# Kernel optimization log

Hardware: AMD Instinct MI355X
Metric: run time of the kernel (lower is better)

Reference implementation:

```python
import jax, jax.numpy as jnp
import numpy as np

N_NODES = 100000
N_EDGES = 1000000
F_IN = 64
F_HID = 32


def setup_inputs() -> dict:
    key = jax.random.key(0)
    k = jax.random.split(key, 6)
    x = jax.random.normal(k[0], (N_NODES, F_IN), dtype=jnp.float32)
    edge_index = jax.random.randint(k[1], (2, N_EDGES), 0, N_NODES, dtype=jnp.int32)
    # Glorot-ish scaled weights (PyG GCNConv linear has no bias; bias added post-aggregation)
    W1 = jax.random.normal(k[2], (F_IN, F_HID), dtype=jnp.float32) / np.sqrt(F_IN)
    b1 = jax.random.normal(k[3], (F_HID,), dtype=jnp.float32) * 0.01
    W2 = jax.random.normal(k[4], (F_HID, F_IN), dtype=jnp.float32) / np.sqrt(F_HID)
    b2 = jax.random.normal(k[5], (F_IN,), dtype=jnp.float32) * 0.01
    return {"x": x, "edge_index": edge_index, "W1": W1, "b1": b1, "W2": W2, "b2": b2}


def gcn_conv(x, W, b, src, dst, n):
    """PyG GCNConv: h = x @ W; add self-loops; symmetric norm; scatter-add; + bias."""
    h = x @ W  # [N, out]
    ones = jnp.ones(src.shape[0], dtype=h.dtype)
    # degree includes the implicit self-loop (+1 per node)
    deg = jax.ops.segment_sum(ones, dst, num_segments=n) + 1.0  # [N]
    dis = jax.lax.rsqrt(deg)  # deg^{-1/2}
    norm = dis[src] * dis[dst]  # [E]
    agg = jax.ops.segment_sum(h[src] * norm[:, None], dst, num_segments=n)
    # self-loop contribution: norm_ii = deg_i^{-1}
    agg = agg + h * (dis * dis)[:, None]
    return agg + b


def reference(x, edge_index, W1, b1, W2, b2):
    src, dst = edge_index[0], edge_index[1]
    n = x.shape[0]
    h = jax.nn.relu(gcn_conv(x, W1, b1, src, dst, n))
    # dropout is identity in eval mode
    return gcn_conv(h, W2, b2, src, dst, n)
```

## Files before the change

### kernel.cpp

```cpp
#include <hip/hip_runtime.h>
#include <hip/hip_fp16.h>

#define NN 100000
#define NE 1000000
#define FIN 64
#define FHID 32
#define NB 782
#define BNODES 128
#define NCH 256
#define CH ((NE + NCH - 1) / NCH)
#define GEMB ((NN + 31) / 32)

union H8 { __half2 h2[4]; float4 f4; };
union H4 { __half2 h2[2]; float2 f2; };

__global__ __launch_bounds__(256) void k_bhist(const int* __restrict__ dst, int* __restrict__ phist) {
    __shared__ int lh[NB];
    for (int i = threadIdx.x; i < NB; i += 256) lh[i] = 0;
    __syncthreads();
    int k = blockIdx.x;
    int e0 = k * CH, e1 = min(e0 + CH, NE);
    for (int e = e0 + threadIdx.x; e < e1; e += 256) atomicAdd(&lh[dst[e] >> 7], 1);
    __syncthreads();
    for (int b = threadIdx.x; b < NB; b += 256) phist[(size_t)k * NB + b] = lh[b];
}

__global__ __launch_bounds__(256) void k_bscan(int* __restrict__ phist, int* __restrict__ btot) {
    int b = blockIdx.x;
    int k = threadIdx.x;
    int v = phist[(size_t)k * NB + b];
    int lane = k & 63, wv = k >> 6;
    int incl = v;
#pragma unroll
    for (int s = 1; s < 64; s <<= 1) {
        int t = __shfl_up(incl, s, 64);
        if (lane >= s) incl += t;
    }
    __shared__ int wt[4];
    if (lane == 63) wt[wv] = incl;
    __syncthreads();
    int add = 0;
#pragma unroll
    for (int w = 0; w < 4; ++w) add += (w < wv) ? wt[w] : 0;
    phist[(size_t)k * NB + b] = add + incl - v;
    if (k == 255) btot[b] = add + incl;
}

__global__ __launch_bounds__(1024) void k_bbase(const int* __restrict__ btot, int* __restrict__ bbase,
                                                int* __restrict__ off) {
    __shared__ int s[1024];
    int b = threadIdx.x;
    int v = (b < NB) ? btot[b] : 0;
    s[b] = v;
    __syncthreads();
    for (int d = 1; d < 1024; d <<= 1) {
        int t = (b >= d) ? s[b - d] : 0;
        __syncthreads();
        s[b] += t;
        __syncthreads();
    }
    if (b < NB) bbase[b] = s[b] - v;
    if (b == 0) { bbase[NB] = NE; off[NN] = NE; }
}

__global__ __launch_bounds__(256) void k_scatter_gemm1(const int* __restrict__ ei,
                                                       const int* __restrict__ phist,
                                                       const int* __restrict__ bbase,
                                                       int* __restrict__ ebuf,
                                                       const float* __restrict__ x,
                                                       const float* __restrict__ W1,
                                                       __half* __restrict__ h1) {
    int r = blockIdx.x;
    bool issc;
    int id;
    if (r < 2 * NCH) { issc = !(r & 1); id = r >> 1; }
    else             { issc = false;    id = r - NCH; }
    if (issc) {
        __shared__ int lh[NB];
        __shared__ int lbase[NB];
        int k = id;
        for (int b = threadIdx.x; b < NB; b += 256) {
            lh[b] = 0;
            lbase[b] = bbase[b] + phist[(size_t)k * NB + b];
        }
        __syncthreads();
        int e0 = k * CH, e1 = min(e0 + CH, NE);
        for (int e = e0 + threadIdx.x; e < e1; e += 256) {
            int s = ei[e], d = ei[NE + e];
            int bb = d >> 7;
            int rr = atomicAdd(&lh[bb], 1);
            ebuf[lbase[bb] + rr] = s * BNODES + (d & 127);
        }
        return;
    }
    __shared__ float Wl[FIN * FHID];
    for (int t = threadIdx.x; t < FIN * FHID / 4; t += 256)
        reinterpret_cast<float4*>(Wl)[t] = reinterpret_cast<const float4*>(W1)[t];
    __syncthreads();
    int row = id * 32 + (threadIdx.x >> 3);
    int l = threadIdx.x & 7;
    if (row >= NN) return;
    const float4* xr = reinterpret_cast<const float4*>(x + (size_t)row * FIN);
    float4 acc = make_float4(0.f, 0.f, 0.f, 0.f);
#pragma unroll
    for (int k4 = 0; k4 < FIN / 4; ++k4) {
        float4 a4 = xr[k4];
#pragma unroll
        for (int j = 0; j < 4; ++j) {
            float a = j == 0 ? a4.x : j == 1 ? a4.y : j == 2 ? a4.z : a4.w;
            const float4 wv = *reinterpret_cast<const float4*>(Wl + (k4 * 4 + j) * FHID + l * 4);
            acc.x += a * wv.x; acc.y += a * wv.y; acc.z += a * wv.z; acc.w += a * wv.w;
        }
    }
    H4 u;
    u.h2[0] = __floats2half2_rn(acc.x, acc.y);
    u.h2[1] = __floats2half2_rn(acc.z, acc.w);
    *reinterpret_cast<float2*>(h1 + (size_t)row * FHID + l * 4) = u.f2;
}

__global__ __launch_bounds__(256) void k_csr(const int* __restrict__ ebuf, const int* __restrict__ bbase,
                                             int* __restrict__ off, float* __restrict__ dis,
                                             int* __restrict__ csr, __half* __restrict__ h1) {
    __shared__ int nh[BNODES];
    __shared__ int ofl[BNODES];
    __shared__ float sdis[BNODES];
    int b = blockIdx.x;
    int n0 = b * BNODES;
    int ebeg = bbase[b], eend = bbase[b + 1];
    int ld = threadIdx.x;
    if (ld < BNODES) nh[ld] = 0;
    __syncthreads();
    for (int e = ebeg + threadIdx.x; e < eend; e += 256) atomicAdd(&nh[ebuf[e] & 127], 1);
    __syncthreads();
    int dval = (ld < BNODES) ? nh[ld] : 0;
    if (ld < BNODES) ofl[ld] = dval;
    __syncthreads();
    for (int s = 1; s < BNODES; s <<= 1) {
        int t = 0;
        if (ld < BNODES && ld >= s) t = ofl[ld - s];
        __syncthreads();
        if (ld < BNODES) ofl[ld] += t;
        __syncthreads();
    }
    if (ld < BNODES) {
        ofl[ld] -= dval;
        float dv = rsqrtf((float)dval + 1.0f);
        sdis[ld] = dv;
        int n = n0 + ld;
        if (n < NN) {
            off[n] = ebeg + ofl[ld];
            dis[n] = dv;
        }
        nh[ld] = 0;
    }
    __syncthreads();
    for (int e = ebeg + threadIdx.x; e < eend; e += 256) {
        int v = ebuf[e];
        int ldd = v & 127;
        int r = atomicAdd(&nh[ldd], 1);
        csr[ebeg + ofl[ldd] + r] = v >> 7;
    }
    int i = ld >> 1, part = ld & 1;
    int n = n0 + i;
    if (n < NN) {
        float dv = sdis[i];
        float4* pr = reinterpret_cast<float4*>(h1 + (size_t)n * FHID + part * 16);
#pragma unroll
        for (int j = 0; j < 2; ++j) {
            float4 v4 = pr[j];
            __half2* hp = reinterpret_cast<__half2*>(&v4);
#pragma unroll
            for (int u = 0; u < 4; ++u) {
                float2 f = __half22float2(hp[u]);
                hp[u] = __floats2half2_rn(f.x * dv, f.y * dv);
            }
            pr[j] = v4;
        }
    }
}

__global__ __launch_bounds__(256) void k_gather1(const int* __restrict__ off, const int* __restrict__ csr,
                                                 const float* __restrict__ dis,
                                                 const __half* __restrict__ h, const float* __restrict__ bias,
                                                 __half* __restrict__ out) {
    int t = blockIdx.x * 256 + threadIdx.x;
    int n = t >> 4;
    int l = t & 15;
    int q = l >> 2, c = l & 3;
    float dn = dis[n];
    int beg = off[n], end = off[n + 1];
    float acc[8] = {0.f, 0.f, 0.f, 0.f, 0.f, 0.f, 0.f, 0.f};
    int p = beg + q;
    int s = (p < end) ? csr[p] : 0;
    for (; p < end; p += 4) {
        int scur = s;
        if (p + 4 < end) s = csr[p + 4];
        float4 v = *reinterpret_cast<const float4*>(h + (size_t)scur * FHID + c * 8);
        const __half2* hp = reinterpret_cast<const __half2*>(&v);
#pragma unroll
        for (int j = 0; j < 4; ++j) {
            float2 f = __half22float2(hp[j]);
            acc[2 * j] += f.x;
            acc[2 * j + 1] += f.y;
        }
    }
#pragma unroll
    for (int j = 0; j < 8; ++j) {
        acc[j] += __shfl_xor(acc[j], 4);
        acc[j] += __shfl_xor(acc[j], 8);
    }
    if (q == 0) {
        float4 sv = *reinterpret_cast<const float4*>(h + (size_t)n * FHID + c * 8);
        const __half2* sp = reinterpret_cast<const __half2*>(&sv);
#pragma unroll
        for (int j = 0; j < 4; ++j) {
            float2 f = __half22float2(sp[j]);
            acc[2 * j] += f.x;
            acc[2 * j + 1] += f.y;
        }
        const float4 b0 = *reinterpret_cast<const float4*>(bias + c * 8);
        const float4 b1v = *reinterpret_cast<const float4*>(bias + c * 8 + 4);
        float bb[8] = {b0.x, b0.y, b0.z, b0.w, b1v.x, b1v.y, b1v.z, b1v.w};
        H8 o;
#pragma unroll
        for (int j = 0; j < 4; ++j) {
            float v0 = dn * acc[2 * j] + bb[2 * j];
            float v1 = dn * acc[2 * j + 1] + bb[2 * j + 1];
            v0 = v0 > 0.f ? v0 : 0.f;
            v1 = v1 > 0.f ? v1 : 0.f;
            o.h2[j] = __floats2half2_rn(dn * v0, dn * v1);
        }
        *reinterpret_cast<float4*>(out + (size_t)n * FHID + c * 8) = o.f4;
    }
}

__global__ __launch_bounds__(256) void k_gather_mm(const int* __restrict__ off, const int* __restrict__ csr,
                                                   const float* __restrict__ dis,
                                                   const __half* __restrict__ h, const float* __restrict__ W2,
                                                   const float* __restrict__ b2, float* __restrict__ out) {
    __shared__ float WL[FHID * FIN];
    __shared__ float aggL[16 * 36];
    for (int t = threadIdx.x; t < FHID * FIN / 4; t += 256)
        reinterpret_cast<float4*>(WL)[t] = reinterpret_cast<const float4*>(W2)[t];

    int i = threadIdx.x >> 4;
    int l = threadIdx.x & 15;
    int q = l >> 2, c = l & 3;
    int n = blockIdx.x * 16 + i;
    {
        float dn = dis[n];
        int beg = off[n], end = off[n + 1];
        float acc[8] = {0.f, 0.f, 0.f, 0.f, 0.f, 0.f, 0.f, 0.f};
        int p = beg + q;
        int s = (p < end) ? csr[p] : 0;
        for (; p < end; p += 4) {
            int scur = s;
            if (p + 4 < end) s = csr[p + 4];
            float4 v = *reinterpret_cast<const float4*>(h + (size_t)scur * FHID + c * 8);
            const __half2* hp = reinterpret_cast<const __half2*>(&v);
#pragma unroll
            for (int j = 0; j < 4; ++j) {
                float2 f = __half22float2(hp[j]);
                acc[2 * j] += f.x;
                acc[2 * j + 1] += f.y;
            }
        }
#pragma unroll
        for (int j = 0; j < 8; ++j) {
            acc[j] += __shfl_xor(acc[j], 4);
            acc[j] += __shfl_xor(acc[j], 8);
        }
        if (q == 0) {
            float4 sv = *reinterpret_cast<const float4*>(h + (size_t)n * FHID + c * 8);
            const __half2* sp = reinterpret_cast<const __half2*>(&sv);
            float* ar = aggL + i * 36 + c * 8;
#pragma unroll
            for (int j = 0; j < 4; ++j) {
                float2 f = __half22float2(sp[j]);
                ar[2 * j] = dn * (acc[2 * j] + f.x);
                ar[2 * j + 1] = dn * (acc[2 * j + 1] + f.y);
            }
        }
    }
    __syncthreads();

    int r = threadIdx.x >> 4;
    int n2 = blockIdx.x * 16 + r;
    int c0 = (threadIdx.x & 15) * 4;
    float4 a0 = *reinterpret_cast<const float4*>(b2 + c0);
    const float* ag = aggL + r * 36;
#pragma unroll
    for (int k = 0; k < FHID; ++k) {
        float a = ag[k];
        const float4 wv = *reinterpret_cast<const float4*>(WL + k * FIN + c0);
        a0.x += a * wv.x; a0.y += a * wv.y; a0.z += a * wv.z; a0.w += a * wv.w;
    }
    *reinterpret_cast<float4*>(out + (size_t)n2 * FIN + c0) = a0;
}

extern "C" void kernel_launch(void* const* d_in, const int* in_sizes, int n_in,
                              void* d_out, int out_size, void* d_ws, size_t ws_size,
                              hipStream_t stream) {
    const float* x  = (const float*)d_in[0];
    const int*   ei = (const int*)d_in[1];
    const float* W1 = (const float*)d_in[2];
    const float* b1 = (const float*)d_in[3];
    const float* W2 = (const float*)d_in[4];
    const float* b2 = (const float*)d_in[5];
    float* out = (float*)d_out;

    char* w = (char*)d_ws;
    auto align = [](size_t v) { return (v + 255) & ~(size_t)255; };
    int*    phist = (int*)w;    w += align((size_t)NCH * NB * 4);
    int*    btot  = (int*)w;    w += align((size_t)NB * 4);
    int*    bbase = (int*)w;    w += align((size_t)(NB + 1) * 4);
    int*    ebuf  = (int*)w;    w += align((size_t)NE * 4);
    int*    off   = (int*)w;    w += align((size_t)(NN + 1) * 4);
    float*  dis   = (float*)w;  w += align((size_t)NN * 4);
    int*    csr   = (int*)w;    w += align((size_t)NE * 4);
    __half* h1    = (__half*)w; w += align((size_t)NN * FHID * 2);
    __half* hbuf  = (__half*)w; w += align((size_t)NN * FHID * 2);

    const int* dst = ei + NE;
    k_bhist<<<NCH, 256, 0, stream>>>(dst, phist);
    k_bscan<<<NB, 256, 0, stream>>>(phist, btot);
    k_bbase<<<1, 1024, 0, stream>>>(btot, bbase, off);
    k_scatter_gemm1<<<NCH + GEMB, 256, 0, stream>>>(ei, phist, bbase, ebuf, x, W1, h1);
    k_csr<<<NB, 256, 0, stream>>>(ebuf, bbase, off, dis, csr, h1);
    k_gather1<<<(NN * 16) / 256, 256, 0, stream>>>(off, csr, dis, h1, b1, hbuf);
    k_gather_mm<<<NN / 16, 256, 0, stream>>>(off, csr, dis, hbuf, W2, b2, out);
}
```

Baseline: 95.51 us.

## Split hidden features into two half-width planes and gather each separately

Stores the hidden features as two 16-wide fp16 planes, so each gather pass reads a 3.2 MB table that is more likely to stay resident in cache. Each of the two gather layers now runs once per plane, using a templated kernel with nontemporal loads of the index array. The second-layer matmul moves into its own kernel, which reads the aggregated fp16 planes. This doubles the number of passes over the CSR index array, adds launches and an extra intermediate buffer, and rounds the layer-2 aggregate to fp16 before the matmul.

```diff
diff --git a/kernel.cpp b/kernel.cpp
--- a/kernel.cpp
+++ b/kernel.cpp
@@ -5,11 +5,15 @@
 #define NE 1000000
 #define FIN 64
 #define FHID 32
+#define FH 16
 #define NB 782
 #define BNODES 128
 #define NCH 256
 #define CH ((NE + NCH - 1) / NCH)
 #define GEMB ((NN + 31) / 32)
+
+typedef float f4v __attribute__((ext_vector_type(4)));
+typedef float f2v __attribute__((ext_vector_type(2)));
 
 union H8 { __half2 h2[4]; float4 f4; };
 union H4 { __half2 h2[2]; float2 f2; };
@@ -69,7 +73,8 @@
                                                        int* __restrict__ ebuf,
                                                        const float* __restrict__ x,
                                                        const float* __restrict__ W1,
-                                                       __half* __restrict__ h1) {
+                                                       __half* __restrict__ h1A,
+                                                       __half* __restrict__ h1B) {
     int r = blockIdx.x;
     bool issc;
     int id;
@@ -115,12 +120,14 @@
     H4 u;
     u.h2[0] = __floats2half2_rn(acc.x, acc.y);
     u.h2[1] = __floats2half2_rn(acc.z, acc.w);
-    *reinterpret_cast<float2*>(h1 + (size_t)row * FHID + l * 4) = u.f2;
+    __half* hb = (l < 4) ? h1A : h1B;
+    *reinterpret_cast<float2*>(hb + (size_t)row * FH + (l & 3) * 4) = u.f2;
 }
 
 __global__ __launch_bounds__(256) void k_csr(const int* __restrict__ ebuf, const int* __restrict__ bbase,
                                              int* __restrict__ off, float* __restrict__ dis,
-                                             int* __restrict__ csr, __half* __restrict__ h1) {
+                                             int* __restrict__ csr, __half* __restrict__ h1A,
+                                             __half* __restrict__ h1B) {
     __shared__ int nh[BNODES];
     __shared__ int ofl[BNODES];
     __shared__ float sdis[BNODES];
@@ -160,11 +167,12 @@
         int r = atomicAdd(&nh[ldd], 1);
         csr[ebeg + ofl[ldd] + r] = v >> 7;
     }
-    int i = ld >> 1, part = ld & 1;
+    int i = ld >> 1, half = ld & 1;
     int n = n0 + i;
     if (n < NN) {
         float dv = sdis[i];
-        float4* pr = reinterpret_cast<float4*>(h1 + (size_t)n * FHID + part * 16);
+        __half* hb = half ? h1B : h1A;
+        float4* pr = reinterpret_cast<float4*>(hb + (size_t)n * FH);
 #pragma unroll
         for (int j = 0; j < 2; ++j) {
             float4 v4 = pr[j];
@@ -179,123 +187,114 @@
     }
 }
 
-__global__ __launch_bounds__(256) void k_gather1(const int* __restrict__ off, const int* __restrict__ csr,
-                                                 const float* __restrict__ dis,
-                                                 const __half* __restrict__ h, const float* __restrict__ bias,
-                                                 __half* __restrict__ out) {
+template <int RELU>
+__global__ __launch_bounds__(256) void k_gather(const int* __restrict__ off, const int* __restrict__ csr,
+                                                const float* __restrict__ dis,
+                                                const __half* __restrict__ hin,
+                                                const float* __restrict__ bias,
+                                                __half* __restrict__ out) {
     int t = blockIdx.x * 256 + threadIdx.x;
     int n = t >> 4;
     int l = t & 15;
     int q = l >> 2, c = l & 3;
     float dn = dis[n];
     int beg = off[n], end = off[n + 1];
-    float acc[8] = {0.f, 0.f, 0.f, 0.f, 0.f, 0.f, 0.f, 0.f};
+    float acc[4] = {0.f, 0.f, 0.f, 0.f};
     int p = beg + q;
-    int s = (p < end) ? csr[p] : 0;
+    int s = (p < end) ? __builtin_nontemporal_load(csr + p) : 0;
     for (; p < end; p += 4) {
         int scur = s;
-        if (p + 4 < end) s = csr[p + 4];
-        float4 v = *reinterpret_cast<const float4*>(h + (size_t)scur * FHID + c * 8);
+        if (p + 4 < end) s = __builtin_nontemporal_load(csr + p + 4);
+        float2 v = *reinterpret_cast<const float2*>(hin + (size_t)scur * FH + c * 4);
         const __half2* hp = reinterpret_cast<const __half2*>(&v);
-#pragma unroll
-        for (int j = 0; j < 4; ++j) {
-            float2 f = __half22float2(hp[j]);
-            acc[2 * j] += f.x;
-            acc[2 * j + 1] += f.y;
-        }
-    }
-#pragma unroll
-    for (int j = 0; j < 8; ++j) {
+        float2 f0 = __half22float2(hp[0]);
+        float2 f1 = __half22float2(hp[1]);
+        acc[0] += f0.x; acc[1] += f0.y; acc[2] += f1.x; acc[3] += f1.y;
+    }
+#pragma unroll
+    for (int j = 0; j < 4; ++j) {
         acc[j] += __shfl_xor(acc[j], 4);
         acc[j] += __shfl_xor(acc[j], 8);
     }
     if (q == 0) {
-        float4 sv = *reinterpret_cast<const float4*>(h + (size_t)n * FHID + c * 8);
+        float2 sv = *reinterpret_cast<const float2*>(hin + (size_t)n * FH + c * 4);
         const __half2* sp = reinterpret_cast<const __half2*>(&sv);
-#pragma unroll
-        for (int j = 0; j < 4; ++j) {
-            float2 f = __half22float2(sp[j]);
-            acc[2 * j] += f.x;
-            acc[2 * j + 1] += f.y;
-        }
-        const float4 b0 = *reinterpret_cast<const float4*>(bias + c * 8);
-        const float4 b1v = *reinterpret_cast<const float4*>(bias + c * 8 + 4);
-        float bb[8] = {b0.x, b0.y, b0.z, b0.w, b1v.x, b1v.y, b1v.z, b1v.w};
-        H8 o;
-#pragma unroll
-        for (int j = 0; j < 4; ++j) {
-            float v0 = dn * acc[2 * j] + bb[2 * j];
-            float v1 = dn * acc[2 * j + 1] + bb[2 * j + 1];
-            v0 = v0 > 0.f ? v0 : 0.f;
-            v1 = v1 > 0.f ? v1 : 0.f;
-            o.h2[j] = __floats2half2_rn(dn * v0, dn * v1);
-        }
-        *reinterpret_cast<float4*>(out + (size_t)n * FHID + c * 8) = o.f4;
-    }
-}
-
-__global__ __launch_bounds__(256) void k_gather_mm(const int* __restrict__ off, const int* __restrict__ csr,
-                                                   const float* __restrict__ dis,
-                                                   const __half* __restrict__ h, const float* __restrict__ W2,
-                                                   const float* __restrict__ b2, float* __restrict__ out) {
+        float2 s0 = __half22float2(sp[0]);
+        float2 s1 = __half22float2(sp[1]);
+        acc[0] += s0.x; acc[1] += s0.y; acc[2] += s1.x; acc[3] += s1.y;
+        float r[4];
+        if (RELU) {
+            const float4 bb = *reinterpret_cast<const float4*>(bias + c * 4);
+            float pre[4] = {dn * acc[0] + bb.x, dn * acc[1] + bb.y,
+                            dn * acc[2] + bb.z, dn * acc[3] + bb.w};
+#pragma unroll
+            for (int j = 0; j < 4; ++j) {
+                float v2 = pre[j] > 0.f ? pre[j] : 0.f;
+                r[j] = dn * v2;
+            }
+        } else {
+#pragma unroll
+            for (int j = 0; j < 4; ++j) r[j] = dn * acc[j];
+        }
+        H4 o;
+        o.h2[0] = __floats2half2_rn(r[0], r[1]);
+        o.h2[1] = __floats2half2_rn(r[2], r[3]);
+        __builtin_nontemporal_store(*reinterpret_cast<const f2v*>(&o.f2),
+                                    reinterpret_cast<f2v*>(out + (size_t)n * FH + c * 4));
+    }
+}
+
+__global__ __launch_bounds__(256) void k_mm2(const __half* __restrict__ aggA, const __half* __restrict__ aggB,
+                                             const float* __restrict__ W2, const float* __restrict__ b2,
+                                             float* __restrict__ out) {
     __shared__ float WL[FHID * FIN];
-    __shared__ float aggL[16 * 36];
     for (int t = threadIdx.x; t < FHID * FIN / 4; t += 256)
         reinterpret_cast<float4*>(WL)[t] = reinterpret_cast<const float4*>(W2)[t];
-
-    int i = threadIdx.x >> 4;
-    int l = threadIdx.x & 15;
-    int q = l >> 2, c = l & 3;
-    int n = blockIdx.x * 16 + i;
+    __syncthreads();
+    int row = blockIdx.x * 32 + (threadIdx.x >> 3);
+    int l = threadIdx.x & 7;
+    int c0 = l * 8;
+    float a[32];
     {
-        float dn = dis[n];
-        int beg = off[n], end = off[n + 1];
-        float acc[8] = {0.f, 0.f, 0.f, 0.f, 0.f, 0.f, 0.f, 0.f};
-        int p = beg + q;
-        int s = (p < end) ? csr[p] : 0;
-        for (; p < end; p += 4) {
-            int scur = s;
-            if (p + 4 < end) s = csr[p + 4];
-            float4 v = *reinterpret_cast<const float4*>(h + (size_t)scur * FHID + c * 8);
-            const __half2* hp = reinterpret_cast<const __half2*>(&v);
+        const float4* pa = reinterpret_cast<const float4*>(aggA + (size_t)row * FH);
+        const float4* pb = reinterpret_cast<const float4*>(aggB + (size_t)row * FH);
+#pragma unroll
+        for (int h = 0; h < 2; ++h) {
+            float4 v4 = pa[h];
+            const __half2* hp = reinterpret_cast<const __half2*>(&v4);
 #pragma unroll
             for (int j = 0; j < 4; ++j) {
                 float2 f = __half22float2(hp[j]);
-                acc[2 * j] += f.x;
-                acc[2 * j + 1] += f.y;
+                a[h * 8 + 2 * j] = f.x;
+                a[h * 8 + 2 * j + 1] = f.y;
             }
         }
 #pragma unroll
-        for (int j = 0; j < 8; ++j) {
-            acc[j] += __shfl_xor(acc[j], 4);
-            acc[j] += __shfl_xor(acc[j], 8);
-        }
-        if (q == 0) {
-            float4 sv = *reinterpret_cast<const float4*>(h + (size_t)n * FHID + c * 8);
-            const __half2* sp = reinterpret_cast<const __half2*>(&sv);
-            float* ar = aggL + i * 36 + c * 8;
+        for (int h = 0; h < 2; ++h) {
+            float4 v4 = pb[h];
+            const __half2* hp = reinterpret_cast<const __half2*>(&v4);
 #pragma unroll
             for (int j = 0; j < 4; ++j) {
-                float2 f = __half22float2(sp[j]);
-                ar[2 * j] = dn * (acc[2 * j] + f.x);
-                ar[2 * j + 1] = dn * (acc[2 * j + 1] + f.y);
+                float2 f = __half22float2(hp[j]);
+                a[16 + h * 8 + 2 * j] = f.x;
+                a[16 + h * 8 + 2 * j + 1] = f.y;
             }
         }
     }
-    __syncthreads();
-
-    int r = threadIdx.x >> 4;
-    int n2 = blockIdx.x * 16 + r;
-    int c0 = (threadIdx.x & 15) * 4;
-    float4 a0 = *reinterpret_cast<const float4*>(b2 + c0);
-    const float* ag = aggL + r * 36;
+    float4 acc0 = *reinterpret_cast<const float4*>(b2 + c0);
+    float4 acc1 = *reinterpret_cast<const float4*>(b2 + c0 + 4);
 #pragma unroll
     for (int k = 0; k < FHID; ++k) {
-        float a = ag[k];
-        const float4 wv = *reinterpret_cast<const float4*>(WL + k * FIN + c0);
-        a0.x += a * wv.x; a0.y += a * wv.y; a0.z += a * wv.z; a0.w += a * wv.w;
-    }
-    *reinterpret_cast<float4*>(out + (size_t)n2 * FIN + c0) = a0;
+        float av = a[k];
+        const float* wr = WL + k * FIN + c0;
+        const float4 w0 = *reinterpret_cast<const float4*>(wr);
+        const float4 w1 = *reinterpret_cast<const float4*>(wr + 4);
+        acc0.x += av * w0.x; acc0.y += av * w0.y; acc0.z += av * w0.z; acc0.w += av * w0.w;
+        acc1.x += av * w1.x; acc1.y += av * w1.y; acc1.z += av * w1.z; acc1.w += av * w1.w;
+    }
+    float* o = out + (size_t)row * FIN + c0;
+    __builtin_nontemporal_store(*reinterpret_cast<const f4v*>(&acc0), reinterpret_cast<f4v*>(o));
+    __builtin_nontemporal_store(*reinterpret_cast<const f4v*>(&acc1), reinterpret_cast<f4v*>(o + 4));
 }
 
 extern "C" void kernel_launch(void* const* d_in, const int* in_sizes, int n_in,
@@ -318,15 +317,22 @@
     int*    off   = (int*)w;    w += align((size_t)(NN + 1) * 4);
     float*  dis   = (float*)w;  w += align((size_t)NN * 4);
     int*    csr   = (int*)w;    w += align((size_t)NE * 4);
-    __half* h1    = (__half*)w; w += align((size_t)NN * FHID * 2);
-    __half* hbuf  = (__half*)w; w += align((size_t)NN * FHID * 2);
+    __half* h1A   = (__half*)w; w += align((size_t)NN * FH * 2);
+    __half* h1B   = (__half*)w; w += align((size_t)NN * FH * 2);
+    __half* hbA   = (__half*)w; w += align((size_t)NN * FH * 2);
+    __half* hbB   = (__half*)w; w += align((size_t)NN * FH * 2);
+    __half* agA   = (__half*)w; w += align((size_t)NN * FH * 2);
+    __half* agB   = (__half*)w; w += align((size_t)NN * FH * 2);
 
     const int* dst = ei + NE;
     k_bhist<<<NCH, 256, 0, stream>>>(dst, phist);
     k_bscan<<<NB, 256, 0, stream>>>(phist, btot);
     k_bbase<<<1, 1024, 0, stream>>>(btot, bbase, off);
-    k_scatter_gemm1<<<NCH + GEMB, 256, 0, stream>>>(ei, phist, bbase, ebuf, x, W1, h1);
-    k_csr<<<NB, 256, 0, stream>>>(ebuf, bbase, off, dis, csr, h1);
-    k_gather1<<<(NN * 16) / 256, 256, 0, stream>>>(off, csr, dis, h1, b1, hbuf);
-    k_gather_mm<<<NN / 16, 256, 0, stream>>>(off, csr, dis, hbuf, W2, b2, out);
-}
+    k_scatter_gemm1<<<NCH + GEMB, 256, 0, stream>>>(ei, phist, bbase, ebuf, x, W1, h1A, h1B);
+    k_csr<<<NB, 256, 0, stream>>>(ebuf, bbase, off, dis, csr, h1A, h1B);
+    k_gather<1><<<(NN * 16) / 256, 256, 0, stream>>>(off, csr, dis, h1A, b1, hbA);
+    k_gather<1><<<(NN * 16) / 256, 256, 0, stream>>>(off, csr, dis, h1B, b1 + FH, hbB);
+    k_gather<0><<<(NN * 16) / 256, 256, 0, stream>>>(off, csr, dis, hbA, nullptr, agA);
+    k_gather<0><<<(NN * 16) / 256, 256, 0, stream>>>(off, csr, dis, hbB, nullptr, agB);
+    k_mm2<<<GEMB, 256, 0, stream>>>(agA, agB, W2, b2, out);
+}
```

Result: slower. 127.4 us (+33.4%).
